# Optimization experiments

Measured on AMD Instinct MI355X. Metric: run time of the kernel, lower is better.

## Reference

```python
import jax, jax.numpy as jnp
import numpy as np

B, S, D = 2, 1024, 2048
H, G, DK, DV = 16, 4, 128, 128
E, K, F = 8, 2, 4096
EPS = 1e-6


def _rms_norm(x, w):
    return x * jax.lax.rsqrt(jnp.mean(x * x, axis=-1, keepdims=True) + EPS) * w


def _rope(x):
    # x: [B, S, h, d]; rotate-half RoPE with base 10000
    d = x.shape[-1]
    half = d // 2
    inv_freq = 1.0 / (10000.0 ** (jnp.arange(half, dtype=jnp.float32) / half))
    ang = jnp.arange(x.shape[1], dtype=jnp.float32)[:, None] * inv_freq[None, :]  # [S, half]
    cos = jnp.cos(ang)[None, :, None, :]
    sin = jnp.sin(ang)[None, :, None, :]
    x1, x2 = x[..., :half], x[..., half:]
    return jnp.concatenate([x1 * cos - x2 * sin, x1 * sin + x2 * cos], axis=-1)


def setup_inputs() -> dict:
    key = jax.random.key(0)
    ks = jax.random.split(key, 10)
    s = lambda *shape: 1.0 / np.sqrt(shape[-2] if len(shape) > 1 else shape[0])
    inp = {
        "x": jax.random.normal(ks[0], (B, S, D), jnp.float32),
        "ln1_w": jnp.ones((D,), jnp.float32),
        "Wq": jax.random.normal(ks[1], (D, H * DK), jnp.float32) * (D ** -0.5),
        "Wk": jax.random.normal(ks[2], (D, G * DK), jnp.float32) * (D ** -0.5),
        "Wv": jax.random.normal(ks[3], (D, G * DV), jnp.float32) * (D ** -0.5),
        "Wo": jax.random.normal(ks[4], (H * DV, D), jnp.float32) * ((H * DV) ** -0.5),
        "ln2_w": jnp.ones((D,), jnp.float32),
        "Wr": jax.random.normal(ks[5], (D, E), jnp.float32) * (D ** -0.5),
        "W1": jax.random.normal(ks[6], (E, D, F), jnp.float32) * (D ** -0.5),
        "W2": jax.random.normal(ks[7], (E, F, D), jnp.float32) * (F ** -0.5),
    }
    return inp


def reference(x, ln1_w, Wq, Wk, Wv, Wo, ln2_w, Wr, W1, W2):
    # --- GQA attention (pre-norm, residual) ---
    h = _rms_norm(x, ln1_w)
    q = (h @ Wq).reshape(B, S, H, DK)
    k = (h @ Wk).reshape(B, S, G, DK)
    v = (h @ Wv).reshape(B, S, G, DV)
    q = _rope(q)
    k = _rope(k)
    # expand KV groups to all heads: each group serves H // G query heads
    rep = H // G
    k = jnp.repeat(k, rep, axis=2)  # [B, S, H, DK]
    v = jnp.repeat(v, rep, axis=2)  # [B, S, H, DV]
    scores = jnp.einsum("bshd,bthd->bhst", q, k) * (DK ** -0.5)  # [B,H,S,S]
    causal = jnp.tril(jnp.ones((S, S), bool))
    scores = jnp.where(causal[None, None], scores, jnp.finfo(scores.dtype).min)
    probs = jax.nn.softmax(scores, axis=-1)
    attn = jnp.einsum("bhst,bthd->bshd", probs, v).reshape(B, S, H * DV)
    x = x + attn @ Wo

    # --- top-k MoE MLP (pre-norm, residual) ---
    h = _rms_norm(x, ln2_w)
    t = h.reshape(B * S, D)  # tokens
    logits = t @ Wr  # [T, E]
    top_vals, top_idx = jax.lax.top_k(logits, K)
    gates = jax.nn.softmax(top_vals, axis=-1)  # [T, K]
    # dense combine weights [T, E] (zero for non-selected experts)
    comb = jnp.zeros((B * S, E), t.dtype)
    comb = comb.at[jnp.arange(B * S)[:, None], top_idx].set(gates)
    # dense all-expert compute (reference form of the grouped GEMM)
    mid = jax.nn.silu(jnp.einsum("td,edf->tef", t, W1))  # [T, E, F]
    out_e = jnp.einsum("tef,efd->ted", mid, W2)          # [T, E, D]
    moe = jnp.einsum("te,ted->td", comb, out_e).reshape(B, S, D)
    return x + moe
```

## Files before the change

### kernel.cpp

```cpp
#include <hip/hip_runtime.h>

typedef unsigned short u16;
typedef __attribute__((ext_vector_type(8))) short bf16x8;
typedef __attribute__((ext_vector_type(4))) float f32x4;

__device__ __forceinline__ u16 f2bf(float f) {
  union { float f; unsigned u; } v; v.f = f;
  unsigned r = (v.u + 0x7fffu + ((v.u >> 16) & 1u)) >> 16;
  return (u16)r;
}
__device__ __forceinline__ float bf2f(u16 u) {
  union { unsigned u; float f; } v; v.u = ((unsigned)u) << 16;
  return v.f;
}
__device__ __forceinline__ void split2(float f, u16& hi, u16& lo) {
  hi = f2bf(f);
  lo = f2bf(f - bf2f(hi));
}

typedef const unsigned int __attribute__((address_space(1)))* gptr_t;
typedef unsigned int __attribute__((address_space(3)))* lptr_t;

__device__ __forceinline__ void gl16(const u16* g, u16* l) {
#if __has_builtin(__builtin_amdgcn_global_load_lds)
  __builtin_amdgcn_global_load_lds((gptr_t)g, (lptr_t)l, 16, 0, 0);
#else
  *reinterpret_cast<uint4*>(l) = *reinterpret_cast<const uint4*>(g);
#endif
}

__device__ __forceinline__ void mf_bf16(const u16* __restrict__ sA,
    const u16* __restrict__ sB, f32x4 (&acc)[4][4], int wm, int wn, int lr, int lk) {
  bf16x8 a[4], b[4];
#pragma unroll
  for (int i = 0; i < 4; i++) {
    a[i] = *reinterpret_cast<const bf16x8*>(&sA[(wm + i * 16 + lr) * 32 + lk]);
    b[i] = *reinterpret_cast<const bf16x8*>(&sB[(wn + i * 16 + lr) * 32 + lk]);
  }
#pragma unroll
  for (int i = 0; i < 4; i++)
#pragma unroll
    for (int j = 0; j < 4; j++)
      acc[i][j] = __builtin_amdgcn_mfma_f32_16x16x32_bf16(a[i], b[j], acc[i][j], 0, 0, 0);
}

__device__ __forceinline__ void mf_hilo(const u16* __restrict__ sAhp,
    const u16* __restrict__ sAlp, const u16* __restrict__ sBhp,
    const u16* __restrict__ sBlp, f32x4 (&acc)[4][4], int wm, int wn, int lr, int lk) {
  bf16x8 ah[4], al[4], bh[4], bl[4];
#pragma unroll
  for (int i = 0; i < 4; i++) {
    ah[i] = *reinterpret_cast<const bf16x8*>(&sAhp[(wm + i * 16 + lr) * 32 + lk]);
    al[i] = *reinterpret_cast<const bf16x8*>(&sAlp[(wm + i * 16 + lr) * 32 + lk]);
    bh[i] = *reinterpret_cast<const bf16x8*>(&sBhp[(wn + i * 16 + lr) * 32 + lk]);
    bl[i] = *reinterpret_cast<const bf16x8*>(&sBlp[(wn + i * 16 + lr) * 32 + lk]);
  }
#pragma unroll
  for (int i = 0; i < 4; i++)
#pragma unroll
    for (int j = 0; j < 4; j++) {
      f32x4 t = acc[i][j];
      t = __builtin_amdgcn_mfma_f32_16x16x32_bf16(al[i], bh[j], t, 0, 0, 0);
      t = __builtin_amdgcn_mfma_f32_16x16x32_bf16(ah[i], bl[j], t, 0, 0, 0);
      t = __builtin_amdgcn_mfma_f32_16x16x32_bf16(ah[i], bh[j], t, 0, 0, 0);
      acc[i][j] = t;
    }
}

#define HILO_PREAMBLE \
  __shared__ __align__(16) u16 sAh[2][4096], sAl[2][4096], sBh[2][4096], sBl[2][4096]; \
  int tid = threadIdx.x, lane = tid & 63; \
  int wm = ((tid >> 6) & 1) << 6, wn = (tid >> 7) << 6; \
  int lr = lane & 15, lk = (lane >> 4) << 3; \
  int er = (lane >> 4) << 2, ec = lane & 15; \
  int r = tid >> 2, c = (tid & 3) << 3; \
  int so = r * 32 + c, so2 = so + 2048; \
  f32x4 acc[4][4] = {};

#define STAGE_HILO(buf) \
  gl16(pAh + ko, &sAh[buf][so]); gl16(pAh2 + ko, &sAh[buf][so2]); \
  gl16(pAl + ko, &sAl[buf][so]); gl16(pAl2 + ko, &sAl[buf][so2]); \
  gl16(pBh + ko, &sBh[buf][so]); gl16(pBh2 + ko, &sBh[buf][so2]); \
  gl16(pBl + ko, &sBl[buf][so]); gl16(pBl2 + ko, &sBl[buf][so2]);

#define BF16_PREAMBLE \
  __shared__ __align__(16) u16 sA[2][4096], sB[2][4096]; \
  int tid = threadIdx.x, lane = tid & 63; \
  int wm = ((tid >> 6) & 1) << 6, wn = (tid >> 7) << 6; \
  int lr = lane & 15, lk = (lane >> 4) << 3; \
  int er = (lane >> 4) << 2, ec = lane & 15; \
  int r = tid >> 2, c = (tid & 3) << 3; \
  int so = r * 32 + c, so2 = so + 2048; \
  f32x4 acc[4][4] = {};

#define STAGE_AB(buf) \
  gl16(pA + ko, &sA[buf][so]); gl16(pA2 + ko, &sA[buf][so2]); \
  gl16(pB + ko, &sB[buf][so]); gl16(pB2 + ko, &sB[buf][so2]);

__global__ __launch_bounds__(256) void convt_bf16(const float* __restrict__ W,
    u16* __restrict__ T, int K, int N) {
  __shared__ float t[64][33];
  long eo = (long)blockIdx.z * K * N;
  int k0 = blockIdx.y << 6, n0 = blockIdx.x << 5;
  int tid = threadIdx.x;
  int r = tid >> 3, cc = (tid & 7) << 2;
  const float* src = W + eo + (long)(k0 + r) * N + n0 + cc;
  float4 a = *reinterpret_cast<const float4*>(src);
  float4 b = *reinterpret_cast<const float4*>(src + (long)32 * N);
  t[r][cc] = a.x; t[r][cc + 1] = a.y; t[r][cc + 2] = a.z; t[r][cc + 3] = a.w;
  t[r + 32][cc] = b.x; t[r + 32][cc + 1] = b.y; t[r + 32][cc + 2] = b.z; t[r + 32][cc + 3] = b.w;
  __syncthreads();
  int n = tid >> 3, kc = (tid & 7) << 3;
  __align__(16) u16 h[8];
#pragma unroll
  for (int i = 0; i < 8; i++) h[i] = f2bf(t[kc + i][n]);
  *reinterpret_cast<uint4*>(&T[eo + (long)(n0 + n) * K + k0 + kc]) =
      *reinterpret_cast<uint4*>(h);
}

__global__ __launch_bounds__(256) void convt_split(const float* __restrict__ W,
    u16* __restrict__ Thi, u16* __restrict__ Tlo, int K, int N) {
  __shared__ float t[64][33];
  int k0 = blockIdx.y << 6, n0 = blockIdx.x << 5;
  int tid = threadIdx.x;
  int r = tid >> 3, cc = (tid & 7) << 2;
  const float* src = W + (long)(k0 + r) * N + n0 + cc;
  float4 a = *reinterpret_cast<const float4*>(src);
  float4 b = *reinterpret_cast<const float4*>(src + (long)32 * N);
  t[r][cc] = a.x; t[r][cc + 1] = a.y; t[r][cc + 2] = a.z; t[r][cc + 3] = a.w;
  t[r + 32][cc] = b.x; t[r + 32][cc + 1] = b.y; t[r + 32][cc + 2] = b.z; t[r + 32][cc + 3] = b.w;
  __syncthreads();
  int n = tid >> 3, kc = (tid & 7) << 3;
  __align__(16) u16 h[8], l[8];
#pragma unroll
  for (int i = 0; i < 8; i++) split2(t[kc + i][n], h[i], l[i]);
  long o = (long)(n0 + n) * K + k0 + kc;
  *reinterpret_cast<uint4*>(&Thi[o]) = *reinterpret_cast<uint4*>(h);
  *reinterpret_cast<uint4*>(&Tlo[o]) = *reinterpret_cast<uint4*>(l);
}


__global__ __launch_bounds__(256) void rmsnorm_split(const float* __restrict__ x,
    const float* __restrict__ w, u16* __restrict__ ohi, u16* __restrict__ olo) {
  __shared__ float lbuf[4];
  int tid = threadIdx.x;
  long base = (long)blockIdx.x * 2048;
  float4 v0 = *reinterpret_cast<const float4*>(&x[base + tid * 8]);
  float4 v1 = *reinterpret_cast<const float4*>(&x[base + tid * 8 + 4]);
  float ss = v0.x * v0.x + v0.y * v0.y + v0.z * v0.z + v0.w * v0.w +
             v1.x * v1.x + v1.y * v1.y + v1.z * v1.z + v1.w * v1.w;
  for (int off = 32; off; off >>= 1) ss += __shfl_down(ss, off);
  if ((tid & 63) == 0) lbuf[tid >> 6] = ss;
  __syncthreads();
  float tot = lbuf[0] + lbuf[1] + lbuf[2] + lbuf[3];
  float scale = 1.0f / sqrtf(tot * (1.0f / 2048.0f) + 1e-6f);
  float4 w0 = *reinterpret_cast<const float4*>(&w[tid * 8]);
  float4 w1 = *reinterpret_cast<const float4*>(&w[tid * 8 + 4]);
  float f[8] = {v0.x * scale * w0.x, v0.y * scale * w0.y, v0.z * scale * w0.z,
                v0.w * scale * w0.w, v1.x * scale * w1.x, v1.y * scale * w1.y,
                v1.z * scale * w1.z, v1.w * scale * w1.w};
  __align__(16) u16 h[8], l[8];
#pragma unroll
  for (int i = 0; i < 8; i++) split2(f[i], h[i], l[i]);
  *reinterpret_cast<uint4*>(&ohi[base + tid * 8]) = *reinterpret_cast<uint4*>(h);
  *reinterpret_cast<uint4*>(&olo[base + tid * 8]) = *reinterpret_cast<uint4*>(l);
}

__global__ __launch_bounds__(256) void rmsnorm_bf16(const float* __restrict__ x,
    const float* __restrict__ w, u16* __restrict__ o) {
  __shared__ float lbuf[4];
  int tid = threadIdx.x;
  long base = (long)blockIdx.x * 2048;
  float4 v0 = *reinterpret_cast<const float4*>(&x[base + tid * 8]);
  float4 v1 = *reinterpret_cast<const float4*>(&x[base + tid * 8 + 4]);
  float ss = v0.x * v0.x + v0.y * v0.y + v0.z * v0.z + v0.w * v0.w +
             v1.x * v1.x + v1.y * v1.y + v1.z * v1.z + v1.w * v1.w;
  for (int off = 32; off; off >>= 1) ss += __shfl_down(ss, off);
  if ((tid & 63) == 0) lbuf[tid >> 6] = ss;
  __syncthreads();
  float tot = lbuf[0] + lbuf[1] + lbuf[2] + lbuf[3];
  float scale = 1.0f / sqrtf(tot * (1.0f / 2048.0f) + 1e-6f);
  float4 w0 = *reinterpret_cast<const float4*>(&w[tid * 8]);
  float4 w1 = *reinterpret_cast<const float4*>(&w[tid * 8 + 4]);
  ushort4 o0, o1;
  o0.x = f2bf(v0.x * scale * w0.x); o0.y = f2bf(v0.y * scale * w0.y);
  o0.z = f2bf(v0.z * scale * w0.z); o0.w = f2bf(v0.w * scale * w0.w);
  o1.x = f2bf(v1.x * scale * w1.x); o1.y = f2bf(v1.y * scale * w1.y);
  o1.z = f2bf(v1.z * scale * w1.z); o1.w = f2bf(v1.w * scale * w1.w);
  *reinterpret_cast<ushort4*>(&o[base + tid * 8]) = o0;
  *reinterpret_cast<ushort4*>(&o[base + tid * 8 + 4]) = o1;
}

__global__ __launch_bounds__(256) void rope2_split(const float* __restrict__ x0,
    const float* __restrict__ x1, int hshift, int hmask, long ld, long colbase,
    u16* __restrict__ ohi, u16* __restrict__ olo) {
  int unit = blockIdx.x * 4 + (threadIdx.x >> 6);
  int lane = threadIdx.x & 63;
  int s = (unit >> hshift) & 1023;
  long src = (long)(unit >> hshift) * ld + colbase + ((long)(unit & hmask) << 7);
  float a1 = x0[src + lane] + x1[src + lane];
  float a2 = x0[src + lane + 64] + x1[src + lane + 64];
  float ang = (float)s * exp2f((float)lane * (-13.287712379549449f / 64.0f));
  float sn, cs;
  sincosf(ang, &sn, &cs);
  long o = (long)unit * 128 + lane;
  u16 hh, ll;
  split2(a1 * cs - a2 * sn, hh, ll);
  ohi[o] = hh; olo[o] = ll;
  split2(a1 * sn + a2 * cs, hh, ll);
  ohi[o + 64] = hh; olo[o + 64] = ll;
}

__global__ __launch_bounds__(256) void transpose2_split(const float* __restrict__ in0,
    const float* __restrict__ in1, long ld, long bstride, u16* __restrict__ ohi,
    u16* __restrict__ olo, int R, int C) {
  __shared__ float tile[32][33];
  long bi = (long)blockIdx.z * bstride;
  long bo = (long)blockIdx.z * R * C;
  int r0 = blockIdx.y * 32, c0 = blockIdx.x * 32;
  int r = threadIdx.x >> 5, c = threadIdx.x & 31;
#pragma unroll
  for (int i = 0; i < 4; i++) {
    long a = bi + (long)(r0 + r + i * 8) * ld + c0 + c;
    tile[r + i * 8][c] = in0[a] + in1[a];
  }
  __syncthreads();
#pragma unroll
  for (int i = 0; i < 4; i++) {
    u16 hh, ll;
    split2(tile[c][r + i * 8], hh, ll);
    long o = bo + (long)(c0 + r + i * 8) * R + r0 + c;
    ohi[o] = hh; olo[o] = ll;
  }
}

__global__ __launch_bounds__(256) void softmax_hilo(u16* __restrict__ ph,
    u16* __restrict__ pl) {
  __shared__ float lbuf[4];
  long row = blockIdx.x;
  int q = (int)(row & 1023);
  int tid = threadIdx.x;
  int valid = q + 1;
  int pend = (q & ~127) + 128;
  int t0 = tid * 4;
  long base = row * 1024 + t0;
  ushort4 vh = *reinterpret_cast<ushort4*>(&ph[base]);
  ushort4 vl = *reinterpret_cast<ushort4*>(&pl[base]);
  float v[4] = {bf2f(vh.x) + bf2f(vl.x), bf2f(vh.y) + bf2f(vl.y),
                bf2f(vh.z) + bf2f(vl.z), bf2f(vh.w) + bf2f(vl.w)};
  float mx = -1e30f;
#pragma unroll
  for (int i = 0; i < 4; i++) {
    if (t0 + i >= valid) v[i] = -1e30f;
    mx = fmaxf(mx, v[i]);
  }
  for (int off = 32; off; off >>= 1) mx = fmaxf(mx, __shfl_down(mx, off));
  if ((tid & 63) == 0) lbuf[tid >> 6] = mx;
  __syncthreads();
  float m = fmaxf(fmaxf(lbuf[0], lbuf[1]), fmaxf(lbuf[2], lbuf[3]));
  __syncthreads();
  float sum = 0.0f;
#pragma unroll
  for (int i = 0; i < 4; i++) {
    float e = (t0 + i < valid) ? expf(v[i] - m) : 0.0f;
    v[i] = e;
    sum += e;
  }
  for (int off = 32; off; off >>= 1) sum += __shfl_down(sum, off);
  if ((tid & 63) == 0) lbuf[tid >> 6] = sum;
  __syncthreads();
  float inv = 1.0f / (lbuf[0] + lbuf[1] + lbuf[2] + lbuf[3]);
  if (t0 < pend) {
    ushort4 oh, ol;
    u16 hh, ll;
    split2(v[0] * inv, hh, ll); oh.x = hh; ol.x = ll;
    split2(v[1] * inv, hh, ll); oh.y = hh; ol.y = ll;
    split2(v[2] * inv, hh, ll); oh.z = hh; ol.z = ll;
    split2(v[3] * inv, hh, ll); oh.w = hh; ol.w = ll;
    *reinterpret_cast<ushort4*>(&ph[base]) = oh;
    *reinterpret_cast<ushort4*>(&pl[base]) = ol;
  }
}

__global__ __launch_bounds__(256) void split_attn(const float* __restrict__ a,
    u16* __restrict__ ohi, u16* __restrict__ olo) {
  long i = ((long)blockIdx.x * 256 + threadIdx.x) * 8;
  float4 v0 = *reinterpret_cast<const float4*>(&a[i]);
  float4 v1 = *reinterpret_cast<const float4*>(&a[i + 4]);
  float f[8] = {v0.x, v0.y, v0.z, v0.w, v1.x, v1.y, v1.z, v1.w};
  __align__(16) u16 h[8], l[8];
#pragma unroll
  for (int j = 0; j < 8; j++) split2(f[j], h[j], l[j]);
  *reinterpret_cast<uint4*>(&ohi[i]) = *reinterpret_cast<uint4*>(h);
  *reinterpret_cast<uint4*>(&olo[i]) = *reinterpret_cast<uint4*>(l);
}

__global__ __launch_bounds__(256) void router_kernel(const float* __restrict__ xo,
    const float* __restrict__ w, const float* __restrict__ Wr,
    int* __restrict__ tok_e, float* __restrict__ tok_g, int* __restrict__ counts) {
  __shared__ float lbuf[32];
  int tid = threadIdx.x;
  long base = (long)blockIdx.x * 2048;
  float4 v0 = *reinterpret_cast<const float4*>(&xo[base + tid * 8]);
  float4 v1 = *reinterpret_cast<const float4*>(&xo[base + tid * 8 + 4]);
  float ss = v0.x * v0.x + v0.y * v0.y + v0.z * v0.z + v0.w * v0.w +
             v1.x * v1.x + v1.y * v1.y + v1.z * v1.z + v1.w * v1.w;
  for (int off = 32; off; off >>= 1) ss += __shfl_down(ss, off);
  if ((tid & 63) == 0) lbuf[tid >> 6] = ss;
  __syncthreads();
  float tot = lbuf[0] + lbuf[1] + lbuf[2] + lbuf[3];
  float scale = 1.0f / sqrtf(tot * (1.0f / 2048.0f) + 1e-6f);
  __syncthreads();
  float4 w0 = *reinterpret_cast<const float4*>(&w[tid * 8]);
  float4 w1 = *reinterpret_cast<const float4*>(&w[tid * 8 + 4]);
  float h[8] = {v0.x * scale * w0.x, v0.y * scale * w0.y, v0.z * scale * w0.z,
                v0.w * scale * w0.w, v1.x * scale * w1.x, v1.y * scale * w1.y,
                v1.z * scale * w1.z, v1.w * scale * w1.w};
  float part[8] = {0, 0, 0, 0, 0, 0, 0, 0};
#pragma unroll
  for (int j = 0; j < 8; j++) {
    const float* wr = Wr + (long)(tid * 8 + j) * 8;
    float4 a = *reinterpret_cast<const float4*>(wr);
    float4 b = *reinterpret_cast<const float4*>(wr + 4);
    part[0] += h[j] * a.x; part[1] += h[j] * a.y;
    part[2] += h[j] * a.z; part[3] += h[j] * a.w;
    part[4] += h[j] * b.x; part[5] += h[j] * b.y;
    part[6] += h[j] * b.z; part[7] += h[j] * b.w;
  }
#pragma unroll
  for (int e = 0; e < 8; e++) {
    float s = part[e];
    for (int off = 32; off; off >>= 1) s += __shfl_down(s, off);
    if ((tid & 63) == 0) lbuf[(tid >> 6) * 8 + e] = s;
  }
  __syncthreads();
  if (tid == 0) {
    float lg[8];
#pragma unroll
    for (int e = 0; e < 8; e++)
      lg[e] = lbuf[e] + lbuf[8 + e] + lbuf[16 + e] + lbuf[24 + e];
    int e1 = 0;
    for (int e = 1; e < 8; e++) if (lg[e] > lg[e1]) e1 = e;
    int e2 = -1;
    for (int e = 0; e < 8; e++) if (e != e1 && (e2 < 0 || lg[e] > lg[e2])) e2 = e;
    float ex = __expf(lg[e2] - lg[e1]);
    float g1 = 1.0f / (1.0f + ex);
    tok_e[blockIdx.x * 2] = e1; tok_e[blockIdx.x * 2 + 1] = e2;
    tok_g[blockIdx.x * 2] = g1; tok_g[blockIdx.x * 2 + 1] = 1.0f - g1;
    atomicAdd(&counts[e1], 1);
    atomicAdd(&counts[e2], 1);
  }
}

__global__ void scan8(const int* __restrict__ counts, int* __restrict__ offsets,
                      int* __restrict__ cursor) {
  if (threadIdx.x == 0) {
    int off = 0;
    for (int e = 0; e < 8; e++) { offsets[e] = off; off += counts[e]; cursor[e] = 0; }
  }
}

__global__ __launch_bounds__(256) void fill_lists(const int* __restrict__ tok_e,
    const float* __restrict__ tok_g, const int* __restrict__ offsets,
    int* __restrict__ cursor, int* __restrict__ ltok, float* __restrict__ lgate) {
  int idx = blockIdx.x * 256 + threadIdx.x;
  int token = idx >> 1;
  int e = tok_e[idx];
  float g = tok_g[idx];
  int pos = atomicAdd(&cursor[e], 1);
  int j = offsets[e] + pos;
  ltok[j] = token;
  lgate[j] = g;
}


__global__ __launch_bounds__(256) void gemm_qkv(
    const u16* __restrict__ Ahi, const u16* __restrict__ Alo,
    const u16* __restrict__ Bhi, const u16* __restrict__ Blo,
    float* __restrict__ C0, float* __restrict__ C1) {
  HILO_PREAMBLE
  int m0 = blockIdx.y << 7, n0 = blockIdx.x << 7;
  long kb = (long)blockIdx.z << 10;
  const u16* pAh = Ahi + (long)(m0 + r) * 2048 + kb + c;  const u16* pAh2 = pAh + 64 * 2048;
  const u16* pAl = Alo + (long)(m0 + r) * 2048 + kb + c;  const u16* pAl2 = pAl + 64 * 2048;
  const u16* pBh = Bhi + (long)(n0 + r) * 2048 + kb + c;  const u16* pBh2 = pBh + 64 * 2048;
  const u16* pBl = Blo + (long)(n0 + r) * 2048 + kb + c;  const u16* pBl2 = pBl + 64 * 2048;
  { int ko = 0; STAGE_HILO(0) }
  __syncthreads();
  int cur = 0;
  for (int k0 = 0; k0 < 1024; k0 += 32) {
    if (k0 + 32 < 1024) { int ko = k0 + 32; STAGE_HILO(cur ^ 1) }
    mf_hilo(sAh[cur], sAl[cur], sBh[cur], sBl[cur], acc, wm, wn, lr, lk);
    __syncthreads();
    cur ^= 1;
  }
  float* C = blockIdx.z ? C1 : C0;
#pragma unroll
  for (int i = 0; i < 4; i++)
#pragma unroll
    for (int j = 0; j < 4; j++)
#pragma unroll
      for (int rr = 0; rr < 4; rr++)
        C[(long)(m0 + wm + i * 16 + er + rr) * 3072 + n0 + wn + j * 16 + ec] =
            acc[i][j][rr];
}

__global__ __launch_bounds__(256) void gemm_wo(
    const u16* __restrict__ Ahi, const u16* __restrict__ Alo,
    const u16* __restrict__ Bhi, const u16* __restrict__ Blo,
    const float* __restrict__ resid, float* __restrict__ C) {
  HILO_PREAMBLE
  int m0 = blockIdx.y << 7, n0 = blockIdx.x << 7;
  long kb = (long)blockIdx.z << 10;
  const u16* pAh = Ahi + (long)(m0 + r) * 2048 + kb + c;  const u16* pAh2 = pAh + 64 * 2048;
  const u16* pAl = Alo + (long)(m0 + r) * 2048 + kb + c;  const u16* pAl2 = pAl + 64 * 2048;
  const u16* pBh = Bhi + (long)(n0 + r) * 2048 + kb + c;  const u16* pBh2 = pBh + 64 * 2048;
  const u16* pBl = Blo + (long)(n0 + r) * 2048 + kb + c;  const u16* pBl2 = pBl + 64 * 2048;
  { int ko = 0; STAGE_HILO(0) }
  __syncthreads();
  int cur = 0;
  for (int k0 = 0; k0 < 1024; k0 += 32) {
    if (k0 + 32 < 1024) { int ko = k0 + 32; STAGE_HILO(cur ^ 1) }
    mf_hilo(sAh[cur], sAl[cur], sBh[cur], sBl[cur], acc, wm, wn, lr, lk);
    __syncthreads();
    cur ^= 1;
  }
  int addres = (blockIdx.z == 0);
#pragma unroll
  for (int i = 0; i < 4; i++)
#pragma unroll
    for (int j = 0; j < 4; j++)
#pragma unroll
      for (int rr = 0; rr < 4; rr++) {
        long idx = (long)(m0 + wm + i * 16 + er + rr) * 2048 + n0 + wn + j * 16 + ec;
        float v = acc[i][j][rr];
        if (addres) v += resid[idx];
        atomicAdd(&C[idx], v);
      }
}

__global__ __launch_bounds__(256) void gemm_qk(
    const u16* __restrict__ qhi, const u16* __restrict__ qlo,
    const u16* __restrict__ khi, const u16* __restrict__ klo,
    u16* __restrict__ schi, u16* __restrict__ sclo) {
  HILO_PREAMBLE
  int idx = blockIdx.x, mi = 0;
  while ((mi + 1) * (mi + 2) / 2 <= idx) mi++;
  int ni = idx - mi * (mi + 1) / 2;
  int bh = blockIdx.y, b = bh >> 4, hd = bh & 15, g = hd >> 2;
  int m0 = mi << 7, n0 = ni << 7;
  const u16* pAh = qhi + (long)b * 2097152 + hd * 128 + (long)(m0 + r) * 2048 + c;
  const u16* pAh2 = pAh + 64 * 2048;
  const u16* pAl = qlo + (long)b * 2097152 + hd * 128 + (long)(m0 + r) * 2048 + c;
  const u16* pAl2 = pAl + 64 * 2048;
  const u16* pBh = khi + (long)b * 524288 + g * 128 + (long)(n0 + r) * 512 + c;
  const u16* pBh2 = pBh + 64 * 512;
  const u16* pBl = klo + (long)b * 524288 + g * 128 + (long)(n0 + r) * 512 + c;
  const u16* pBl2 = pBl + 64 * 512;
  { int ko = 0; STAGE_HILO(0) }
  __syncthreads();
  int cur = 0;
  for (int k0 = 0; k0 < 128; k0 += 32) {
    if (k0 + 32 < 128) { int ko = k0 + 32; STAGE_HILO(cur ^ 1) }
    mf_hilo(sAh[cur], sAl[cur], sBh[cur], sBl[cur], acc, wm, wn, lr, lk);
    __syncthreads();
    cur ^= 1;
  }
  long Cb = (long)bh * 1048576 + (long)m0 * 1024 + n0;
  const float scalef = 0.08838834764831845f;
#pragma unroll
  for (int i = 0; i < 4; i++)
#pragma unroll
    for (int j = 0; j < 4; j++)
#pragma unroll
      for (int rr = 0; rr < 4; rr++) {
        u16 hh, ll;
        split2(acc[i][j][rr] * scalef, hh, ll);
        long o = Cb + (long)(wm + i * 16 + er + rr) * 1024 + wn + j * 16 + ec;
        schi[o] = hh; sclo[o] = ll;
      }
}

__global__ __launch_bounds__(256) void gemm_pv_tri(
    const u16* __restrict__ phi, const u16* __restrict__ plo,
    const u16* __restrict__ vthi, const u16* __restrict__ vtlo,
    float* __restrict__ attnf) {
  HILO_PREAMBLE
  int idx = blockIdx.x, mi = 0;
  while ((mi + 1) * (mi + 2) / 2 <= idx) mi++;
  int ki = idx - mi * (mi + 1) / 2;
  int bh = blockIdx.y, b = bh >> 4, hd = bh & 15, g = hd >> 2;
  int m0 = mi << 7;
  long kb = (long)ki << 7;
  const u16* pAh = phi + (long)bh * 1048576 + (long)(m0 + r) * 1024 + kb + c;
  const u16* pAh2 = pAh + 64 * 1024;
  const u16* pAl = plo + (long)bh * 1048576 + (long)(m0 + r) * 1024 + kb + c;
  const u16* pAl2 = pAl + 64 * 1024;
  const u16* pBh = vthi + (long)(b * 4 + g) * 131072 + (long)r * 1024 + kb + c;
  const u16* pBh2 = pBh + 64 * 1024;
  const u16* pBl = vtlo + (long)(b * 4 + g) * 131072 + (long)r * 1024 + kb + c;
  const u16* pBl2 = pBl + 64 * 1024;
  { int ko = 0; STAGE_HILO(0) }
  __syncthreads();
  int cur = 0;
  for (int k0 = 0; k0 < 128; k0 += 32) {
    if (k0 + 32 < 128) { int ko = k0 + 32; STAGE_HILO(cur ^ 1) }
    mf_hilo(sAh[cur], sAl[cur], sBh[cur], sBl[cur], acc, wm, wn, lr, lk);
    __syncthreads();
    cur ^= 1;
  }
  long Cb = ((long)(b * 1024 + m0) * 16 + hd) * 128;
#pragma unroll
  for (int i = 0; i < 4; i++)
#pragma unroll
    for (int j = 0; j < 4; j++)
#pragma unroll
      for (int rr = 0; rr < 4; rr++)
        atomicAdd(&attnf[Cb + (long)(wm + i * 16 + er + rr) * 2048 + wn + j * 16 + ec],
                  acc[i][j][rr]);
}


__global__ __launch_bounds__(256) void gemm_moe1(const u16* __restrict__ t2,
    const u16* __restrict__ W1T, const int* __restrict__ offsets,
    const int* __restrict__ counts, const int* __restrict__ ltok,
    u16* __restrict__ mid) {
  int e = blockIdx.z;
  int cnt = counts[e];
  int m0 = blockIdx.y << 7;
  if (m0 >= cnt) return;
  BF16_PREAMBLE
  int off = offsets[e];
  int n0 = blockIdx.x << 7;
  int valid = cnt - m0; if (valid > 128) valid = 128;
  int rr0 = (r < valid) ? r : 0;
  int rr1 = (r + 64 < valid) ? (r + 64) : 0;
  const u16* pA = t2 + (long)ltok[off + m0 + rr0] * 2048 + c;
  const u16* pA2 = t2 + (long)ltok[off + m0 + rr1] * 2048 + c;
  const u16* pB = W1T + (long)e * 8388608 + (long)(n0 + r) * 2048 + c;
  const u16* pB2 = pB + 64 * 2048;
  { int ko = 0; STAGE_AB(0) }
  __syncthreads();
  int cur = 0;
  for (int k0 = 0; k0 < 2048; k0 += 32) {
    if (k0 + 32 < 2048) { int ko = k0 + 32; STAGE_AB(cur ^ 1) }
    mf_bf16(sA[cur], sB[cur], acc, wm, wn, lr, lk);
    __syncthreads();
    cur ^= 1;
  }
#pragma unroll
  for (int i = 0; i < 4; i++)
#pragma unroll
    for (int j = 0; j < 4; j++)
#pragma unroll
      for (int rr = 0; rr < 4; rr++) {
        int rowl = wm + i * 16 + er + rr;
        if (rowl < valid) {
          float v = acc[i][j][rr];
          v = v / (1.0f + __expf(-v));
          mid[(long)(off + m0 + rowl) * 4096 + n0 + wn + j * 16 + ec] = f2bf(v);
        }
      }
}

__global__ __launch_bounds__(256) void gemm_moe2(const u16* __restrict__ mid,
    const u16* __restrict__ W2T, const int* __restrict__ offsets,
    const int* __restrict__ counts, const int* __restrict__ ltok,
    const float* __restrict__ lgate, float* __restrict__ out) {
  int e = blockIdx.z;
  int cnt = counts[e];
  int mt = blockIdx.y >> 1, ks = blockIdx.y & 1;
  int m0 = mt << 7;
  if (m0 >= cnt) return;
  BF16_PREAMBLE
  int off = offsets[e];
  int n0 = blockIdx.x << 7;
  long kb = (long)ks << 11;
  int valid = cnt - m0; if (valid > 128) valid = 128;
  int rw0 = off + m0 + ((r < valid) ? r : valid - 1);
  int rw1 = off + m0 + ((r + 64 < valid) ? r + 64 : valid - 1);
  const u16* pA = mid + (long)rw0 * 4096 + kb + c;
  const u16* pA2 = mid + (long)rw1 * 4096 + kb + c;
  const u16* pB = W2T + (long)e * 8388608 + (long)(n0 + r) * 4096 + kb + c;
  const u16* pB2 = pB + 64 * 4096;
  { int ko = 0; STAGE_AB(0) }
  __syncthreads();
  int cur = 0;
  for (int k0 = 0; k0 < 2048; k0 += 32) {
    if (k0 + 32 < 2048) { int ko = k0 + 32; STAGE_AB(cur ^ 1) }
    mf_bf16(sA[cur], sB[cur], acc, wm, wn, lr, lk);
    __syncthreads();
    cur ^= 1;
  }
#pragma unroll
  for (int i = 0; i < 4; i++)
#pragma unroll
    for (int j = 0; j < 4; j++)
#pragma unroll
      for (int rr = 0; rr < 4; rr++) {
        int rowl = wm + i * 16 + er + rr;
        if (rowl < valid) {
          int t = ltok[off + m0 + rowl];
          float g = lgate[off + m0 + rowl];
          atomicAdd(&out[(long)t * 2048 + n0 + wn + j * 16 + ec], g * acc[i][j][rr]);
        }
      }
}

extern "C" void kernel_launch(void* const* d_in, const int* in_sizes, int n_in,
                              void* d_out, int out_size, void* d_ws, size_t ws_size,
                              hipStream_t stream) {
  (void)in_sizes; (void)n_in; (void)out_size; (void)ws_size;
  const float* x   = (const float*)d_in[0];
  const float* ln1 = (const float*)d_in[1];
  const float* Wq  = (const float*)d_in[2];
  const float* Wk  = (const float*)d_in[3];
  const float* Wv  = (const float*)d_in[4];
  const float* Wo  = (const float*)d_in[5];
  const float* ln2 = (const float*)d_in[6];
  const float* Wr  = (const float*)d_in[7];
  const float* W1  = (const float*)d_in[8];
  const float* W2  = (const float*)d_in[9];
  float* out = (float*)d_out;
  char* ws = (char*)d_ws;

  u16* hhi    = (u16*)(ws);
  u16* hlo    = (u16*)(ws + 8388608);
  float* qkv0 = (float*)(ws + 16777216);
  float* qkv1 = (float*)(ws + 41943040);
  u16* wqkvh  = (u16*)(ws + 67108864);
  u16* wqkvl  = (u16*)(ws + 79691776);
  u16* schi   = (u16*)(ws);
  u16* sclo   = (u16*)(ws + 67108864);
  u16* athi   = (u16*)(ws + 134217728);
  u16* atlo   = (u16*)(ws + 142606336);
  u16* qhi    = (u16*)(ws + 150994944);
  u16* qlo    = (u16*)(ws + 159383552);
  float* attnf = (float*)(ws + 150994944);
  u16* khi    = (u16*)(ws + 167772160);
  u16* klo    = (u16*)(ws + 169869312);
  u16* vthi   = (u16*)(ws + 171966464);
  u16* vtlo   = (u16*)(ws + 174063616);
  u16* woh    = (u16*)(ws + 176160768);
  u16* wol    = (u16*)(ws + 184549376);
  u16* wbuf = (u16*)(ws);
  u16* mid  = (u16*)(ws + 134217728);
  u16* t2   = (u16*)(ws + 167772160);
  char* misc = ws + 176160768;
  int*   tok_e   = (int*)misc;
  float* tok_g   = (float*)(misc + 16384);
  int*   ltok    = (int*)(misc + 32768);
  float* lgate   = (float*)(misc + 49152);
  int*   counts  = (int*)(misc + 65536);
  int*   offsets = (int*)(misc + 65600);
  int*   cursor  = (int*)(misc + 65664);

  convt_split<<<dim3(64, 32), 256, 0, stream>>>(Wq, wqkvh, wqkvl, 2048, 2048);
  convt_split<<<dim3(16, 32), 256, 0, stream>>>(Wk, wqkvh + 2048 * 2048,
                                                wqkvl + 2048 * 2048, 2048, 512);
  convt_split<<<dim3(16, 32), 256, 0, stream>>>(Wv, wqkvh + 2560 * 2048,
                                                wqkvl + 2560 * 2048, 2048, 512);
  convt_split<<<dim3(64, 32), 256, 0, stream>>>(Wo, woh, wol, 2048, 2048);

  rmsnorm_split<<<2048, 256, 0, stream>>>(x, ln1, hhi, hlo);
  gemm_qkv<<<dim3(24, 16, 2), 256, 0, stream>>>(hhi, hlo, wqkvh, wqkvl, qkv0, qkv1);
  rope2_split<<<8192, 256, 0, stream>>>(qkv0, qkv1, 4, 15, 3072, 0, qhi, qlo);
  rope2_split<<<2048, 256, 0, stream>>>(qkv0, qkv1, 2, 3, 3072, 2048, khi, klo);
  transpose2_split<<<dim3(16, 32, 2), 256, 0, stream>>>(
      qkv0 + 2560, qkv1 + 2560, 3072, 3145728, vthi, vtlo, 1024, 512);
  gemm_qk<<<dim3(36, 32), 256, 0, stream>>>(qhi, qlo, khi, klo, schi, sclo);
  softmax_hilo<<<32768, 256, 0, stream>>>(schi, sclo);
  hipMemsetAsync(attnf, 0, 16777216, stream);
  gemm_pv_tri<<<dim3(36, 32), 256, 0, stream>>>(schi, sclo, vthi, vtlo, attnf);
  split_attn<<<2048, 256, 0, stream>>>(attnf, athi, atlo);
  hipMemsetAsync(out, 0, 16777216, stream);
  gemm_wo<<<dim3(16, 16, 2), 256, 0, stream>>>(athi, atlo, woh, wol, x, out);

  rmsnorm_bf16<<<2048, 256, 0, stream>>>(out, ln2, t2);
  hipMemsetAsync(counts, 0, 32, stream);
  router_kernel<<<2048, 256, 0, stream>>>(out, ln2, Wr, tok_e, tok_g, counts);
  scan8<<<1, 64, 0, stream>>>(counts, offsets, cursor);
  fill_lists<<<16, 256, 0, stream>>>(tok_e, tok_g, offsets, cursor, ltok, lgate);
  convt_bf16<<<dim3(128, 32, 8), 256, 0, stream>>>(W1, wbuf, 2048, 4096);
  gemm_moe1<<<dim3(32, 16, 8), 256, 0, stream>>>(t2, wbuf, offsets, counts, ltok, mid);
  convt_bf16<<<dim3(64, 64, 8), 256, 0, stream>>>(W2, wbuf, 4096, 2048);
  gemm_moe2<<<dim3(16, 32, 8), 256, 0, stream>>>(mid, wbuf, offsets, counts, ltok,
                                                 lgate, out);
}
```

Baseline: 1.333 ms.

## Fuse expert weight bf16 conversion into MoE GEMMs and rmsnorm into router

The separate transpose-convert passes over W1 and W2, which wrote bf16 copies to a workspace, are removed. The MoE GEMMs now load fp32 weights into registers, convert them to bf16 and store them transposed into shared memory inside the pipelined k-loop. The second rmsnorm is folded into the router kernel, and the split-K in moe2 is dropped so each block runs the full K=4096. This saves the extra round trip through global memory for 128 MB of expert weights, but it doubles the weight bytes each GEMM block reads and adds conversion work and LDS stores on the critical loop. Removing split-K in moe2 also halves its grid size.

```diff
diff --git a/kernel.cpp b/kernel.cpp
--- a/kernel.cpp
+++ b/kernel.cpp
@@ -93,29 +93,27 @@
   int so = r * 32 + c, so2 = so + 2048; \
   f32x4 acc[4][4] = {};
 
-#define STAGE_AB(buf) \
-  gl16(pA + ko, &sA[buf][so]); gl16(pA2 + ko, &sA[buf][so2]); \
-  gl16(pB + ko, &sB[buf][so]); gl16(pB2 + ko, &sB[buf][so2]);
-
-__global__ __launch_bounds__(256) void convt_bf16(const float* __restrict__ W,
-    u16* __restrict__ T, int K, int N) {
-  __shared__ float t[64][33];
-  long eo = (long)blockIdx.z * K * N;
-  int k0 = blockIdx.y << 6, n0 = blockIdx.x << 5;
-  int tid = threadIdx.x;
-  int r = tid >> 3, cc = (tid & 7) << 2;
-  const float* src = W + eo + (long)(k0 + r) * N + n0 + cc;
-  float4 a = *reinterpret_cast<const float4*>(src);
-  float4 b = *reinterpret_cast<const float4*>(src + (long)32 * N);
-  t[r][cc] = a.x; t[r][cc + 1] = a.y; t[r][cc + 2] = a.z; t[r][cc + 3] = a.w;
-  t[r + 32][cc] = b.x; t[r + 32][cc + 1] = b.y; t[r + 32][cc + 2] = b.z; t[r + 32][cc + 3] = b.w;
-  __syncthreads();
-  int n = tid >> 3, kc = (tid & 7) << 3;
-  __align__(16) u16 h[8];
-#pragma unroll
-  for (int i = 0; i < 8; i++) h[i] = f2bf(t[kc + i][n]);
-  *reinterpret_cast<uint4*>(&T[eo + (long)(n0 + n) * K + k0 + kc]) =
-      *reinterpret_cast<uint4*>(h);
+__device__ __forceinline__ void ldB_f32(const float* __restrict__ B, long ld,
+    int k0, int tid, float4 (&rr)[4]) {
+  int n4 = (tid & 31) << 2, k4 = (tid >> 5) << 2;
+  const float* p = B + (long)(k0 + k4) * ld + n4;
+  rr[0] = *reinterpret_cast<const float4*>(p);
+  rr[1] = *reinterpret_cast<const float4*>(p + ld);
+  rr[2] = *reinterpret_cast<const float4*>(p + 2 * ld);
+  rr[3] = *reinterpret_cast<const float4*>(p + 3 * ld);
+}
+__device__ __forceinline__ void stB_bf16(u16* __restrict__ s, int tid,
+    const float4 (&rr)[4]) {
+  int n4 = (tid & 31) << 2, k4 = (tid >> 5) << 2;
+#pragma unroll
+  for (int j = 0; j < 4; j++) {
+    ushort4 o;
+    o.x = f2bf(((const float*)&rr[0])[j]);
+    o.y = f2bf(((const float*)&rr[1])[j]);
+    o.z = f2bf(((const float*)&rr[2])[j]);
+    o.w = f2bf(((const float*)&rr[3])[j]);
+    *reinterpret_cast<ushort4*>(&s[(n4 + j) * 32 + k4]) = o;
+  }
 }
 
 __global__ __launch_bounds__(256) void convt_split(const float* __restrict__ W,
@@ -164,31 +162,6 @@
   for (int i = 0; i < 8; i++) split2(f[i], h[i], l[i]);
   *reinterpret_cast<uint4*>(&ohi[base + tid * 8]) = *reinterpret_cast<uint4*>(h);
   *reinterpret_cast<uint4*>(&olo[base + tid * 8]) = *reinterpret_cast<uint4*>(l);
-}
-
-__global__ __launch_bounds__(256) void rmsnorm_bf16(const float* __restrict__ x,
-    const float* __restrict__ w, u16* __restrict__ o) {
-  __shared__ float lbuf[4];
-  int tid = threadIdx.x;
-  long base = (long)blockIdx.x * 2048;
-  float4 v0 = *reinterpret_cast<const float4*>(&x[base + tid * 8]);
-  float4 v1 = *reinterpret_cast<const float4*>(&x[base + tid * 8 + 4]);
-  float ss = v0.x * v0.x + v0.y * v0.y + v0.z * v0.z + v0.w * v0.w +
-             v1.x * v1.x + v1.y * v1.y + v1.z * v1.z + v1.w * v1.w;
-  for (int off = 32; off; off >>= 1) ss += __shfl_down(ss, off);
-  if ((tid & 63) == 0) lbuf[tid >> 6] = ss;
-  __syncthreads();
-  float tot = lbuf[0] + lbuf[1] + lbuf[2] + lbuf[3];
-  float scale = 1.0f / sqrtf(tot * (1.0f / 2048.0f) + 1e-6f);
-  float4 w0 = *reinterpret_cast<const float4*>(&w[tid * 8]);
-  float4 w1 = *reinterpret_cast<const float4*>(&w[tid * 8 + 4]);
-  ushort4 o0, o1;
-  o0.x = f2bf(v0.x * scale * w0.x); o0.y = f2bf(v0.y * scale * w0.y);
-  o0.z = f2bf(v0.z * scale * w0.z); o0.w = f2bf(v0.w * scale * w0.w);
-  o1.x = f2bf(v1.x * scale * w1.x); o1.y = f2bf(v1.y * scale * w1.y);
-  o1.z = f2bf(v1.z * scale * w1.z); o1.w = f2bf(v1.w * scale * w1.w);
-  *reinterpret_cast<ushort4*>(&o[base + tid * 8]) = o0;
-  *reinterpret_cast<ushort4*>(&o[base + tid * 8 + 4]) = o1;
 }
 
 __global__ __launch_bounds__(256) void rope2_split(const float* __restrict__ x0,
@@ -297,7 +270,8 @@
 
 __global__ __launch_bounds__(256) void router_kernel(const float* __restrict__ xo,
     const float* __restrict__ w, const float* __restrict__ Wr,
-    int* __restrict__ tok_e, float* __restrict__ tok_g, int* __restrict__ counts) {
+    int* __restrict__ tok_e, float* __restrict__ tok_g, int* __restrict__ counts,
+    u16* __restrict__ t2o) {
   __shared__ float lbuf[32];
   int tid = threadIdx.x;
   long base = (long)blockIdx.x * 2048;
@@ -316,6 +290,11 @@
   float h[8] = {v0.x * scale * w0.x, v0.y * scale * w0.y, v0.z * scale * w0.z,
                 v0.w * scale * w0.w, v1.x * scale * w1.x, v1.y * scale * w1.y,
                 v1.z * scale * w1.z, v1.w * scale * w1.w};
+  ushort4 o0, o1;
+  o0.x = f2bf(h[0]); o0.y = f2bf(h[1]); o0.z = f2bf(h[2]); o0.w = f2bf(h[3]);
+  o1.x = f2bf(h[4]); o1.y = f2bf(h[5]); o1.z = f2bf(h[6]); o1.w = f2bf(h[7]);
+  *reinterpret_cast<ushort4*>(&t2o[base + tid * 8]) = o0;
+  *reinterpret_cast<ushort4*>(&t2o[base + tid * 8 + 4]) = o1;
   float part[8] = {0, 0, 0, 0, 0, 0, 0, 0};
 #pragma unroll
   for (int j = 0; j < 8; j++) {
@@ -522,7 +501,7 @@
 
 
 __global__ __launch_bounds__(256) void gemm_moe1(const u16* __restrict__ t2,
-    const u16* __restrict__ W1T, const int* __restrict__ offsets,
+    const float* __restrict__ W1, const int* __restrict__ offsets,
     const int* __restrict__ counts, const int* __restrict__ ltok,
     u16* __restrict__ mid) {
   int e = blockIdx.z;
@@ -537,14 +516,21 @@
   int rr1 = (r + 64 < valid) ? (r + 64) : 0;
   const u16* pA = t2 + (long)ltok[off + m0 + rr0] * 2048 + c;
   const u16* pA2 = t2 + (long)ltok[off + m0 + rr1] * 2048 + c;
-  const u16* pB = W1T + (long)e * 8388608 + (long)(n0 + r) * 2048 + c;
-  const u16* pB2 = pB + 64 * 2048;
-  { int ko = 0; STAGE_AB(0) }
+  const float* Bb = W1 + (long)e * 8388608 + n0;
+  float4 rB[4];
+  ldB_f32(Bb, 4096, 0, tid, rB);
+  { int ko = 0; gl16(pA + ko, &sA[0][so]); gl16(pA2 + ko, &sA[0][so2]); }
+  stB_bf16(sB[0], tid, rB);
   __syncthreads();
   int cur = 0;
   for (int k0 = 0; k0 < 2048; k0 += 32) {
-    if (k0 + 32 < 2048) { int ko = k0 + 32; STAGE_AB(cur ^ 1) }
+    if (k0 + 32 < 2048) {
+      ldB_f32(Bb, 4096, k0 + 32, tid, rB);
+      int ko = k0 + 32;
+      gl16(pA + ko, &sA[cur ^ 1][so]); gl16(pA2 + ko, &sA[cur ^ 1][so2]);
+    }
     mf_bf16(sA[cur], sB[cur], acc, wm, wn, lr, lk);
+    if (k0 + 32 < 2048) stB_bf16(sB[cur ^ 1], tid, rB);
     __syncthreads();
     cur ^= 1;
   }
@@ -564,31 +550,36 @@
 }
 
 __global__ __launch_bounds__(256) void gemm_moe2(const u16* __restrict__ mid,
-    const u16* __restrict__ W2T, const int* __restrict__ offsets,
+    const float* __restrict__ W2, const int* __restrict__ offsets,
     const int* __restrict__ counts, const int* __restrict__ ltok,
     const float* __restrict__ lgate, float* __restrict__ out) {
   int e = blockIdx.z;
   int cnt = counts[e];
-  int mt = blockIdx.y >> 1, ks = blockIdx.y & 1;
-  int m0 = mt << 7;
+  int m0 = blockIdx.y << 7;
   if (m0 >= cnt) return;
   BF16_PREAMBLE
   int off = offsets[e];
   int n0 = blockIdx.x << 7;
-  long kb = (long)ks << 11;
   int valid = cnt - m0; if (valid > 128) valid = 128;
   int rw0 = off + m0 + ((r < valid) ? r : valid - 1);
   int rw1 = off + m0 + ((r + 64 < valid) ? r + 64 : valid - 1);
-  const u16* pA = mid + (long)rw0 * 4096 + kb + c;
-  const u16* pA2 = mid + (long)rw1 * 4096 + kb + c;
-  const u16* pB = W2T + (long)e * 8388608 + (long)(n0 + r) * 4096 + kb + c;
-  const u16* pB2 = pB + 64 * 4096;
-  { int ko = 0; STAGE_AB(0) }
+  const u16* pA = mid + (long)rw0 * 4096 + c;
+  const u16* pA2 = mid + (long)rw1 * 4096 + c;
+  const float* Bb = W2 + (long)e * 8388608 + n0;
+  float4 rB[4];
+  ldB_f32(Bb, 2048, 0, tid, rB);
+  { int ko = 0; gl16(pA + ko, &sA[0][so]); gl16(pA2 + ko, &sA[0][so2]); }
+  stB_bf16(sB[0], tid, rB);
   __syncthreads();
   int cur = 0;
-  for (int k0 = 0; k0 < 2048; k0 += 32) {
-    if (k0 + 32 < 2048) { int ko = k0 + 32; STAGE_AB(cur ^ 1) }
+  for (int k0 = 0; k0 < 4096; k0 += 32) {
+    if (k0 + 32 < 4096) {
+      ldB_f32(Bb, 2048, k0 + 32, tid, rB);
+      int ko = k0 + 32;
+      gl16(pA + ko, &sA[cur ^ 1][so]); gl16(pA2 + ko, &sA[cur ^ 1][so2]);
+    }
     mf_bf16(sA[cur], sB[cur], acc, wm, wn, lr, lk);
+    if (k0 + 32 < 4096) stB_bf16(sB[cur ^ 1], tid, rB);
     __syncthreads();
     cur ^= 1;
   }
@@ -643,7 +634,6 @@
   u16* vtlo   = (u16*)(ws + 174063616);
   u16* woh    = (u16*)(ws + 176160768);
   u16* wol    = (u16*)(ws + 184549376);
-  u16* wbuf = (u16*)(ws);
   u16* mid  = (u16*)(ws + 134217728);
   u16* t2   = (u16*)(ws + 167772160);
   char* misc = ws + 176160768;
@@ -676,14 +666,11 @@
   hipMemsetAsync(out, 0, 16777216, stream);
   gemm_wo<<<dim3(16, 16, 2), 256, 0, stream>>>(athi, atlo, woh, wol, x, out);
 
-  rmsnorm_bf16<<<2048, 256, 0, stream>>>(out, ln2, t2);
   hipMemsetAsync(counts, 0, 32, stream);
-  router_kernel<<<2048, 256, 0, stream>>>(out, ln2, Wr, tok_e, tok_g, counts);
+  router_kernel<<<2048, 256, 0, stream>>>(out, ln2, Wr, tok_e, tok_g, counts, t2);
   scan8<<<1, 64, 0, stream>>>(counts, offsets, cursor);
   fill_lists<<<16, 256, 0, stream>>>(tok_e, tok_g, offsets, cursor, ltok, lgate);
-  convt_bf16<<<dim3(128, 32, 8), 256, 0, stream>>>(W1, wbuf, 2048, 4096);
-  gemm_moe1<<<dim3(32, 16, 8), 256, 0, stream>>>(t2, wbuf, offsets, counts, ltok, mid);
-  convt_bf16<<<dim3(64, 64, 8), 256, 0, stream>>>(W2, wbuf, 4096, 2048);
-  gemm_moe2<<<dim3(16, 32, 8), 256, 0, stream>>>(mid, wbuf, offsets, counts, ltok,
+  gemm_moe1<<<dim3(32, 16, 8), 256, 0, stream>>>(t2, W1, offsets, counts, ltok, mid);
+  gemm_moe2<<<dim3(16, 16, 8), 256, 0, stream>>>(mid, W2, offsets, counts, ltok,
                                                  lgate, out);
 }
```

Result: slower. 1.430 ms (+7.3%).
